# Kernel tuning notes

Measured on AMD Instinct MI355X. Metric: run time of the kernel, lower is better.

The kernel has to match this reference:

```python
import jax, jax.numpy as jnp
import numpy as np

DIM = 1024
HEADS = 16
DIM_HEAD = 64
INNER = HEADS * DIM_HEAD
LN_EPS = 1e-5


def setup_inputs() -> dict:
    key = jax.random.key(0)
    ks = jax.random.split(key, 7)
    b, n = 2, 2048
    x = jax.random.normal(ks[0], (b, n, DIM), dtype=jnp.float32)
    attn_bias = jax.random.normal(ks[1], (HEADS, n, n), dtype=jnp.float32)
    gamma = jnp.ones((DIM,), dtype=jnp.float32)
    beta = jnp.zeros((DIM,), dtype=jnp.float32)
    wq = jax.random.normal(ks[2], (DIM, INNER), dtype=jnp.float32) * (DIM ** -0.5)
    wkv = jax.random.normal(ks[3], (DIM, 2 * INNER), dtype=jnp.float32) * (DIM ** -0.5)
    wo = jax.random.normal(ks[4], (INNER, DIM), dtype=jnp.float32) * (INNER ** -0.5)
    return {"x": x, "attn_bias": attn_bias, "gamma": gamma, "beta": beta,
            "wq": wq, "wkv": wkv, "wo": wo}


def reference(x, attn_bias, gamma, beta, wq, wkv, wo):
    b, n, _ = x.shape
    scale = DIM_HEAD ** -0.5
    # LayerNorm
    mu = jnp.mean(x, axis=-1, keepdims=True)
    var = jnp.var(x, axis=-1, keepdims=True)
    xn = (x - mu) * jax.lax.rsqrt(var + LN_EPS) * gamma + beta
    # QKV projections
    q = xn @ wq                      # [b, n, inner]
    kv = xn @ wkv                    # [b, n, 2*inner]
    k, v = jnp.split(kv, 2, axis=-1)
    split_heads = lambda t: t.reshape(b, n, HEADS, DIM_HEAD).transpose(0, 2, 1, 3)
    q, k, v = map(split_heads, (q, k, v))  # [b, h, n, d]
    q = q * scale
    sim = jnp.einsum('bhid,bhjd->bhij', q, k)
    sim = sim + attn_bias[None]      # broadcast over batch
    causal_mask = jnp.triu(jnp.ones((n, n), dtype=bool), k=1)
    sim = jnp.where(causal_mask, -jnp.finfo(sim.dtype).max, sim)
    attn = jax.nn.softmax(sim, axis=-1)
    out = jnp.einsum('bhij,bhjd->bhid', attn, v)
    out = out.transpose(0, 2, 1, 3).reshape(b, n, INNER)
    return out @ wo
```

## Files before the change

### kernel.cpp

```cpp
#include <hip/hip_runtime.h>
#include <hip/hip_bf16.h>

#define DIM   1024
#define HEADS 16
#define DHEAD 64
#define INNER 1024
#define NSEQ  2048
#define NB    2
#define MROWS (NB * NSEQ)
#define QS    (3 * INNER)

typedef __attribute__((ext_vector_type(8))) short    short8;
typedef __attribute__((ext_vector_type(4))) short    short4v;
typedef __attribute__((ext_vector_type(4))) float    floatx4;
typedef __attribute__((ext_vector_type(8))) _Float16 half8;

#define GLOBAL_AS __attribute__((address_space(1)))
#define LDS_AS    __attribute__((address_space(3)))

static __device__ __forceinline__ short f2h(float f) {
  _Float16 h = (_Float16)f;
  return __builtin_bit_cast(short, h);
}
static __device__ __forceinline__ float h2f(short s) {
  return (float)__builtin_bit_cast(_Float16, s);
}

static __device__ __forceinline__ floatx4 mfma16(short8 a, short8 b, floatx4 c) {
  return __builtin_amdgcn_mfma_f32_16x16x32_f16(
      __builtin_bit_cast(half8, a), __builtin_bit_cast(half8, b), c, 0, 0, 0);
}

__global__ __launch_bounds__(256) void ln_kernel(const float* __restrict__ x,
                                                 const float* __restrict__ gamma,
                                                 const float* __restrict__ beta,
                                                 short* __restrict__ xn) {
  int row = blockIdx.x;
  int t   = threadIdx.x;
  const float4* xr = reinterpret_cast<const float4*>(x + (size_t)row * DIM);
  float4 v = xr[t];
  float s  = v.x + v.y + v.z + v.w;
  float s2 = v.x * v.x + v.y * v.y + v.z * v.z + v.w * v.w;
#pragma unroll
  for (int off = 1; off < 64; off <<= 1) {
    s  += __shfl_xor(s, off);
    s2 += __shfl_xor(s2, off);
  }
  __shared__ float red[8];
  if ((t & 63) == 0) { red[t >> 6] = s; red[(t >> 6) + 4] = s2; }
  __syncthreads();
  s  = red[0] + red[1] + red[2] + red[3];
  s2 = red[4] + red[5] + red[6] + red[7];
  float mu   = s * (1.0f / DIM);
  float var  = s2 * (1.0f / DIM) - mu * mu;
  float rstd = rsqrtf(var + 1e-5f);
  float4 g  = reinterpret_cast<const float4*>(gamma)[t];
  float4 bb = reinterpret_cast<const float4*>(beta)[t];
  short4v o;
  o.x = f2h((v.x - mu) * rstd * g.x + bb.x);
  o.y = f2h((v.y - mu) * rstd * g.y + bb.y);
  o.z = f2h((v.z - mu) * rstd * g.z + bb.z);
  o.w = f2h((v.w - mu) * rstd * g.w + bb.w);
  reinterpret_cast<short4v*>(xn + (size_t)row * DIM)[t] = o;
}

__global__ __launch_bounds__(256) void transpose_f16(const float* __restrict__ w,
                                                     short* __restrict__ wt,
                                                     int Kk, int Nn) {
  __shared__ float tile[32][33];
  int n0 = blockIdx.x * 32, k0 = blockIdx.y * 32;
  int tx = threadIdx.x & 31, ty = threadIdx.x >> 5;
#pragma unroll
  for (int i = 0; i < 32; i += 8)
    tile[ty + i][tx] = w[(size_t)(k0 + ty + i) * Nn + n0 + tx];
  __syncthreads();
#pragma unroll
  for (int i = 0; i < 32; i += 8)
    wt[(size_t)(n0 + ty + i) * Kk + k0 + tx] = f2h(tile[tx][ty + i]);
}

template <bool F32OUT>
__global__ __launch_bounds__(256) void gemm_bt(const short* __restrict__ A,
                                               const short* __restrict__ Bt,
                                               void* __restrict__ Cout,
                                               int Nn, int Kk,
                                               float oscale, float oscale2,
                                               int qsplit) {
  constexpr int BM = 128, BN = 128, BK = 64;
  __shared__ __attribute__((aligned(16))) short As[BM * BK];
  __shared__ __attribute__((aligned(16))) short Bs[BN * BK];
  int bm = blockIdx.x, bn = blockIdx.y;
  int t = threadIdx.x, lane = t & 63, w = t >> 6;
  int l15 = lane & 15, lhi = lane >> 4;
  int wr = w >> 1, wc = w & 1;
  float osc = (bn * BN < qsplit) ? oscale : oscale2;
  floatx4 acc[4][4] = {};
  const short* Ag = A + (size_t)bm * BM * Kk;
  const short* Bg = Bt + (size_t)bn * BN * Kk;

  for (int k0 = 0; k0 < Kk; k0 += BK) {
#pragma unroll
    for (int it = 0; it < 4; ++it) {
      int base = it * 256 + w * 64;
      int idx  = base + lane;
      int row  = idx >> 3, kc = (idx & 7) << 3;
      __builtin_amdgcn_global_load_lds(
          (const GLOBAL_AS unsigned int*)(Ag + (size_t)row * Kk + k0 + kc),
          (LDS_AS unsigned int*)(As + base * 8), 16, 0, 0);
    }
#pragma unroll
    for (int it = 0; it < 4; ++it) {
      int base = it * 256 + w * 64;
      int idx  = base + lane;
      int row  = idx >> 3, kc = (idx & 7) << 3;
      __builtin_amdgcn_global_load_lds(
          (const GLOBAL_AS unsigned int*)(Bg + (size_t)row * Kk + k0 + kc),
          (LDS_AS unsigned int*)(Bs + base * 8), 16, 0, 0);
    }
    __syncthreads();
#pragma unroll
    for (int kc = 0; kc < 2; ++kc) {
      short8 a[4], b[4];
#pragma unroll
      for (int mt = 0; mt < 4; ++mt)
        a[mt] = *reinterpret_cast<const short8*>(
            &As[(wr * 64 + mt * 16 + l15) * BK + lhi * 8 + kc * 32]);
#pragma unroll
      for (int nt = 0; nt < 4; ++nt)
        b[nt] = *reinterpret_cast<const short8*>(
            &Bs[(wc * 64 + nt * 16 + l15) * BK + lhi * 8 + kc * 32]);
#pragma unroll
      for (int mt = 0; mt < 4; ++mt)
#pragma unroll
        for (int nt = 0; nt < 4; ++nt)
          acc[mt][nt] = mfma16(a[mt], b[nt], acc[mt][nt]);
    }
    __syncthreads();
  }

  int row0 = bm * BM + wr * 64;
  int col0 = bn * BN + wc * 64;
#pragma unroll
  for (int mt = 0; mt < 4; ++mt)
#pragma unroll
    for (int nt = 0; nt < 4; ++nt)
#pragma unroll
      for (int r = 0; r < 4; ++r) {
        int row = row0 + mt * 16 + lhi * 4 + r;
        int col = col0 + nt * 16 + l15;
        if (F32OUT)
          ((float*)Cout)[(size_t)row * Nn + col] = acc[mt][nt][r] * osc;
        else
          ((short*)Cout)[(size_t)row * Nn + col] = f2h(acc[mt][nt][r] * osc);
      }
}

__global__ __launch_bounds__(256) void attn_kernel(const short* __restrict__ qkv,
                                                   const float* __restrict__ bias,
                                                   short* __restrict__ Opart,
                                                   float* __restrict__ mlpart) {
  constexpr int LDK = 72;
  __shared__ __attribute__((aligned(16))) short Ks[2][64 * LDK];
  __shared__ __attribute__((aligned(16))) short Vt[2][64 * LDK];
  __shared__ __attribute__((aligned(16))) short Ps[64 * LDK];
  int id = blockIdx.x, h = blockIdx.y, b = blockIdx.z;
  int qt, c;
  if (id < 32)      { c = 0; qt = 31 - id; }
  else if (id < 56) { c = 1; qt = 63 - id; }
  else if (id < 72) { c = 2; qt = 87 - id; }
  else              { c = 3; qt = 103 - id; }
  int tt0 = c * 8;
  int tt1 = (tt0 + 8 < qt + 1) ? (tt0 + 8) : (qt + 1);
  int qb = qt * 64;
  int t = threadIdx.x, lane = t & 63, w = t >> 6;
  int l15 = lane & 15, lhi = lane >> 4;

  const short* qrow =
      qkv + ((size_t)(b * NSEQ + qb + w * 16 + l15)) * QS + h * DHEAD + lhi * 8;
  short8 qf0 = *reinterpret_cast<const short8*>(qrow);
  short8 qf1 = *reinterpret_cast<const short8*>(qrow + 32);

  int krow = t >> 3, kcol = (t & 7) << 3;
  int rr = (t >> 3) * 2, cc = (t & 7) << 3;
  short8 kr0, kr1, vr0, vr1;

  auto issue_kv = [&](int tile) {
    int j0 = tile * 64;
    const short* kp =
        qkv + ((size_t)(b * NSEQ + j0 + krow)) * QS + INNER + h * DHEAD + kcol;
    kr0 = *reinterpret_cast<const short8*>(kp);
    kr1 = *reinterpret_cast<const short8*>(kp + (size_t)32 * QS);
    const short* vp = qkv + ((size_t)(b * NSEQ + j0 + rr)) * QS +
                      2 * INNER + h * DHEAD + cc;
    vr0 = *reinterpret_cast<const short8*>(vp);
    vr1 = *reinterpret_cast<const short8*>(vp + QS);
  };
  auto issue_bias = [&](int tile, floatx4 (&br)[4]) {
    const float* bb =
        bias + ((size_t)h * NSEQ + (qb + w * 16 + lhi * 4)) * NSEQ + tile * 64 + l15;
#pragma unroll
    for (int jt = 0; jt < 4; ++jt)
#pragma unroll
      for (int r = 0; r < 4; ++r)
        br[jt][r] = bb[(size_t)r * NSEQ + jt * 16];
  };
  auto writeKV = [&](int buf) {
    *reinterpret_cast<short8*>(&Ks[buf][krow * LDK + kcol]) = kr0;
    *reinterpret_cast<short8*>(&Ks[buf][(krow + 32) * LDK + kcol]) = kr1;
#pragma unroll
    for (int e = 0; e < 8; ++e) {
      int d  = cc + e;
      int jj = rr ^ (((d >> 3) & 7) << 3);
      unsigned int pk = (unsigned short)vr0[e] |
                        ((unsigned int)(unsigned short)vr1[e] << 16);
      *reinterpret_cast<unsigned int*>(&Vt[buf][d * LDK + jj]) = pk;
    }
  };

  float mrow[4], lrow[4];
  floatx4 oacc[4] = {};
#pragma unroll
  for (int r = 0; r < 4; ++r) { mrow[r] = -1e30f; lrow[r] = 0.f; }

  auto step = [&](int tt, int buf, floatx4 (&br)[4]) {
    if (tt + 1 < tt1) issue_kv(tt + 1);
    __syncthreads();

    floatx4 s[4];
#pragma unroll
    for (int jt = 0; jt < 4; ++jt) s[jt] = br[jt];
    if (tt + 2 < tt1) issue_bias(tt + 2, br);

#pragma unroll
    for (int jt = 0; jt < 4; ++jt) {
      short8 kf0 = *reinterpret_cast<const short8*>(
          &Ks[buf][(jt * 16 + l15) * LDK + lhi * 8]);
      short8 kf1 = *reinterpret_cast<const short8*>(
          &Ks[buf][(jt * 16 + l15) * LDK + lhi * 8 + 32]);
      s[jt] = mfma16(qf0, kf0, s[jt]);
      s[jt] = mfma16(qf1, kf1, s[jt]);
    }

    if (tt == qt) {
#pragma unroll
      for (int jt = 0; jt < 4; ++jt)
#pragma unroll
        for (int r = 0; r < 4; ++r) {
          int iloc = lhi * 4 + r;
          int jloc = jt * 16 + l15;
          if (jloc > w * 16 + iloc) s[jt][r] = -1e30f;
        }
    }

#pragma unroll
    for (int r = 0; r < 4; ++r) {
      float mx = fmaxf(fmaxf(s[0][r], s[1][r]), fmaxf(s[2][r], s[3][r]));
#pragma unroll
      for (int off = 1; off < 16; off <<= 1) mx = fmaxf(mx, __shfl_xor(mx, off));
      float mnew = fmaxf(mrow[r], mx);
      float fac  = __expf(mrow[r] - mnew);
      mrow[r] = mnew;
      float ps = 0.f;
#pragma unroll
      for (int jt = 0; jt < 4; ++jt) {
        float p = __expf(s[jt][r] - mnew);
        s[jt][r] = p;
        ps += p;
      }
#pragma unroll
      for (int off = 1; off < 16; off <<= 1) ps += __shfl_xor(ps, off);
      lrow[r] = lrow[r] * fac + ps;
#pragma unroll
      for (int dt = 0; dt < 4; ++dt) oacc[dt][r] *= fac;
    }

#pragma unroll
    for (int jt = 0; jt < 4; ++jt)
#pragma unroll
      for (int r = 0; r < 4; ++r)
        Ps[(w * 16 + lhi * 4 + r) * LDK + jt * 16 + l15] = f2h(s[jt][r]);

#pragma unroll
    for (int jc = 0; jc < 2; ++jc) {
      short8 pf = *reinterpret_cast<const short8*>(
          &Ps[(w * 16 + l15) * LDK + lhi * 8 + jc * 32]);
#pragma unroll
      for (int dt = 0; dt < 4; ++dt) {
        int dd = dt * 16 + l15;
        int jj = (lhi * 8 + jc * 32) ^ (((dd >> 3) & 7) << 3);
        short8 vf = *reinterpret_cast<const short8*>(&Vt[buf][dd * LDK + jj]);
        oacc[dt] = mfma16(pf, vf, oacc[dt]);
      }
    }

    if (tt + 1 < tt1) writeKV(buf ^ 1);
  };

  floatx4 brA[4], brB[4];
  issue_kv(tt0);
  issue_bias(tt0, brA);
  if (tt0 + 1 < tt1) issue_bias(tt0 + 1, brB);
  writeKV(0);

  int nt = tt1 - tt0;
  for (int i = 0; i < nt; i += 2) {
    step(tt0 + i, 0, brA);
    if (i + 1 < nt) step(tt0 + i + 1, 1, brB);
  }

  size_t p = (size_t)(b * HEADS + h) * 80 + id;
  short* Ob = Opart + p * 4096;
#pragma unroll
  for (int dt = 0; dt < 4; ++dt)
#pragma unroll
    for (int r = 0; r < 4; ++r)
      Ob[(w * 16 + lhi * 4 + r) * 64 + dt * 16 + l15] = f2h(oacc[dt][r]);
  if (l15 == 0) {
#pragma unroll
    for (int r = 0; r < 4; ++r) {
      mlpart[p * 128 + (w * 16 + lhi * 4 + r)] = mrow[r];
      mlpart[p * 128 + 64 + (w * 16 + lhi * 4 + r)] = lrow[r];
    }
  }
}

__global__ __launch_bounds__(256) void attn_combine(const short* __restrict__ Opart,
                                                    const float* __restrict__ mlpart,
                                                    short* __restrict__ o) {
  int qt = blockIdx.x, h = blockIdx.y, b = blockIdx.z;
  int nc = qt / 8 + 1;
  int t = threadIdx.x, row = t >> 2, cg = (t & 3) << 4;
  size_t base = (size_t)(b * HEADS + h) * 80;
  const int idtab[4] = {31, 63, 87, 103};

  float M = -1e30f;
  float mv0 = 0, mv1 = 0, mv2 = 0, mv3 = 0, lv0 = 0, lv1 = 0, lv2 = 0, lv3 = 0;
  {
    size_t p = base + idtab[0] - qt;
    mv0 = mlpart[p * 128 + row]; lv0 = mlpart[p * 128 + 64 + row];
    M = mv0;
  }
  if (nc > 1) { size_t p = base + idtab[1] - qt;
    mv1 = mlpart[p * 128 + row]; lv1 = mlpart[p * 128 + 64 + row]; M = fmaxf(M, mv1); }
  if (nc > 2) { size_t p = base + idtab[2] - qt;
    mv2 = mlpart[p * 128 + row]; lv2 = mlpart[p * 128 + 64 + row]; M = fmaxf(M, mv2); }
  if (nc > 3) { size_t p = base + idtab[3] - qt;
    mv3 = mlpart[p * 128 + row]; lv3 = mlpart[p * 128 + 64 + row]; M = fmaxf(M, mv3); }

  float acc[16] = {};
  float lsum = 0.f;
#pragma unroll
  for (int c2 = 0; c2 < 4; ++c2) {
    if (c2 >= nc) break;
    float mc = (c2 == 0) ? mv0 : (c2 == 1) ? mv1 : (c2 == 2) ? mv2 : mv3;
    float lc = (c2 == 0) ? lv0 : (c2 == 1) ? lv1 : (c2 == 2) ? lv2 : lv3;
    float wgt = __expf(mc - M);
    lsum += wgt * lc;
    size_t p = base + idtab[c2] - qt;
    const short8* Or =
        reinterpret_cast<const short8*>(Opart + p * 4096 + row * 64 + cg);
    short8 a0 = Or[0], a1 = Or[1];
#pragma unroll
    for (int e = 0; e < 8; ++e) {
      acc[e]     += wgt * h2f(a0[e]);
      acc[8 + e] += wgt * h2f(a1[e]);
    }
  }
  float inv = 1.f / lsum;
  short* op = o + ((size_t)(b * NSEQ + qt * 64 + row)) * INNER + h * DHEAD + cg;
  short8 o0, o1;
#pragma unroll
  for (int e = 0; e < 8; ++e) {
    o0[e] = f2h(acc[e] * inv);
    o1[e] = f2h(acc[8 + e] * inv);
  }
  reinterpret_cast<short8*>(op)[0] = o0;
  reinterpret_cast<short8*>(op)[1] = o1;
}

extern "C" void kernel_launch(void* const* d_in, const int* in_sizes, int n_in,
                              void* d_out, int out_size, void* d_ws, size_t ws_size,
                              hipStream_t stream) {
  const float* x     = (const float*)d_in[0];
  const float* bias  = (const float*)d_in[1];
  const float* gamma = (const float*)d_in[2];
  const float* beta  = (const float*)d_in[3];
  const float* wq    = (const float*)d_in[4];
  const float* wkv   = (const float*)d_in[5];
  const float* wo    = (const float*)d_in[6];
  float* out = (float*)d_out;

  char* ws = (char*)d_ws;
  const size_t MB = 1024 * 1024;
  short* xn      = (short*)(ws);
  short* wqkv_t  = (short*)(ws + 8  * MB);
  short* wo_t    = (short*)(ws + 14 * MB);
  short* qkv     = (short*)(ws + 16 * MB);
  short* Opart   = (short*)(ws + 40 * MB);
  float* mlpart  = (float*)(ws + 60 * MB);
  short* ao      = xn;

  ln_kernel<<<MROWS, 256, 0, stream>>>(x, gamma, beta, xn);
  transpose_f16<<<dim3(INNER / 32, DIM / 32), 256, 0, stream>>>(wq, wqkv_t, DIM, INNER);
  transpose_f16<<<dim3(2 * INNER / 32, DIM / 32), 256, 0, stream>>>(
      wkv, wqkv_t + (size_t)1024 * 1024, DIM, 2 * INNER);
  transpose_f16<<<dim3(DIM / 32, INNER / 32), 256, 0, stream>>>(wo, wo_t, INNER, DIM);

  gemm_bt<false><<<dim3(MROWS / 128, QS / 128), 256, 0, stream>>>(
      xn, wqkv_t, qkv, QS, DIM, 0.125f, 1.0f, 1024);

  attn_kernel<<<dim3(80, HEADS, NB), 256, 0, stream>>>(qkv, bias, Opart, mlpart);
  attn_combine<<<dim3(32, HEADS, NB), 256, 0, stream>>>(Opart, mlpart, ao);

  gemm_bt<true><<<dim3(MROWS / 128, DIM / 128), 256, 0, stream>>>(
      ao, wo_t, out, DIM, INNER, 1.0f, 1.0f, 0);
}
```

Baseline: 182.5 us.

## Transpose S=QK^T MFMA so each lane owns one query row in softmax

Swaps the MFMA operand order so the score tile comes out transposed: each lane holds 16 key columns of a single query row. Row max and sum then need only two cross-lane shuffles instead of four per row, and per-row m/l become scalars. Bias loads turn into contiguous float4 vector loads and P stores into short4 vector stores. The cost is four extra shuffles to redistribute the rescale factor to the output accumulator layout.

```diff
diff --git a/kernel.cpp b/kernel.cpp
--- a/kernel.cpp
+++ b/kernel.cpp
@@ -197,12 +197,10 @@
   };
   auto issue_bias = [&](int tile, floatx4 (&br)[4]) {
     const float* bb =
-        bias + ((size_t)h * NSEQ + (qb + w * 16 + lhi * 4)) * NSEQ + tile * 64 + l15;
+        bias + ((size_t)h * NSEQ + (qb + w * 16 + l15)) * NSEQ + tile * 64 + lhi * 4;
 #pragma unroll
     for (int jt = 0; jt < 4; ++jt)
-#pragma unroll
-      for (int r = 0; r < 4; ++r)
-        br[jt][r] = bb[(size_t)r * NSEQ + jt * 16];
+      br[jt] = *reinterpret_cast<const floatx4*>(bb + jt * 16);
   };
   auto writeKV = [&](int buf) {
     *reinterpret_cast<short8*>(&Ks[buf][krow * LDK + kcol]) = kr0;
@@ -217,10 +215,8 @@
     }
   };
 
-  float mrow[4], lrow[4];
+  float m = -1e30f, l = 0.f;
   floatx4 oacc[4] = {};
-#pragma unroll
-  for (int r = 0; r < 4; ++r) { mrow[r] = -1e30f; lrow[r] = 0.f; }
 
   auto step = [&](int tt, int buf, floatx4 (&br)[4]) {
     if (tt + 1 < tt1) issue_kv(tt + 1);
@@ -237,8 +233,8 @@
           &Ks[buf][(jt * 16 + l15) * LDK + lhi * 8]);
       short8 kf1 = *reinterpret_cast<const short8*>(
           &Ks[buf][(jt * 16 + l15) * LDK + lhi * 8 + 32]);
-      s[jt] = mfma16(qf0, kf0, s[jt]);
-      s[jt] = mfma16(qf1, kf1, s[jt]);
+      s[jt] = mfma16(kf0, qf0, s[jt]);
+      s[jt] = mfma16(kf1, qf1, s[jt]);
     }
 
     if (tt == qt) {
@@ -246,39 +242,51 @@
       for (int jt = 0; jt < 4; ++jt)
 #pragma unroll
         for (int r = 0; r < 4; ++r) {
-          int iloc = lhi * 4 + r;
-          int jloc = jt * 16 + l15;
-          if (jloc > w * 16 + iloc) s[jt][r] = -1e30f;
+          int jloc = jt * 16 + lhi * 4 + r;
+          if (jloc > w * 16 + l15) s[jt][r] = -1e30f;
         }
     }
 
-#pragma unroll
-    for (int r = 0; r < 4; ++r) {
-      float mx = fmaxf(fmaxf(s[0][r], s[1][r]), fmaxf(s[2][r], s[3][r]));
-#pragma unroll
-      for (int off = 1; off < 16; off <<= 1) mx = fmaxf(mx, __shfl_xor(mx, off));
-      float mnew = fmaxf(mrow[r], mx);
-      float fac  = __expf(mrow[r] - mnew);
-      mrow[r] = mnew;
-      float ps = 0.f;
-#pragma unroll
-      for (int jt = 0; jt < 4; ++jt) {
-        float p = __expf(s[jt][r] - mnew);
-        s[jt][r] = p;
-        ps += p;
+    float mx = s[0][0];
+#pragma unroll
+    for (int jt = 0; jt < 4; ++jt)
+#pragma unroll
+      for (int r = 0; r < 4; ++r) mx = fmaxf(mx, s[jt][r]);
+    mx = fmaxf(mx, __shfl_xor(mx, 16));
+    mx = fmaxf(mx, __shfl_xor(mx, 32));
+    float mnew = fmaxf(m, mx);
+    float fac  = __expf(m - mnew);
+    m = mnew;
+    float ps = 0.f;
+#pragma unroll
+    for (int jt = 0; jt < 4; ++jt)
+#pragma unroll
+      for (int r = 0; r < 4; ++r) {
+        float pv = __expf(s[jt][r] - mnew);
+        s[jt][r] = pv;
+        ps += pv;
       }
-#pragma unroll
-      for (int off = 1; off < 16; off <<= 1) ps += __shfl_xor(ps, off);
-      lrow[r] = lrow[r] * fac + ps;
-#pragma unroll
-      for (int dt = 0; dt < 4; ++dt) oacc[dt][r] *= fac;
-    }
-
-#pragma unroll
-    for (int jt = 0; jt < 4; ++jt)
-#pragma unroll
-      for (int r = 0; r < 4; ++r)
-        Ps[(w * 16 + lhi * 4 + r) * LDK + jt * 16 + l15] = f2h(s[jt][r]);
+    ps += __shfl_xor(ps, 16);
+    ps += __shfl_xor(ps, 32);
+    l = l * fac + ps;
+
+    float facr[4];
+#pragma unroll
+    for (int r = 0; r < 4; ++r)
+      facr[r] = __shfl(fac, (lane & 48) | (lhi * 4 + r));
+#pragma unroll
+    for (int dt = 0; dt < 4; ++dt)
+#pragma unroll
+      for (int r = 0; r < 4; ++r) oacc[dt][r] *= facr[r];
+
+#pragma unroll
+    for (int jt = 0; jt < 4; ++jt) {
+      short4v pv4;
+      pv4.x = f2h(s[jt][0]); pv4.y = f2h(s[jt][1]);
+      pv4.z = f2h(s[jt][2]); pv4.w = f2h(s[jt][3]);
+      *reinterpret_cast<short4v*>(
+          &Ps[(w * 16 + l15) * LDK + jt * 16 + lhi * 4]) = pv4;
+    }
 
 #pragma unroll
     for (int jc = 0; jc < 2; ++jc) {
@@ -315,12 +323,9 @@
 #pragma unroll
     for (int r = 0; r < 4; ++r)
       Ob[(w * 16 + lhi * 4 + r) * 64 + dt * 16 + l15] = f2h(oacc[dt][r]);
-  if (l15 == 0) {
-#pragma unroll
-    for (int r = 0; r < 4; ++r) {
-      mlpart[p * 128 + (w * 16 + lhi * 4 + r)] = mrow[r];
-      mlpart[p * 128 + 64 + (w * 16 + lhi * 4 + r)] = lrow[r];
-    }
+  if (lhi == 0) {
+    mlpart[p * 128 + w * 16 + l15] = m;
+    mlpart[p * 128 + 64 + w * 16 + l15] = l;
   }
 }
 
```

Measured after the change: 175.0 us. 1.04x faster.
